# Kernel tuning notes

Hardware: AMD Instinct MI355X
Metric: run time of the kernel (lower is better)

Reference implementation:

```python
import jax, jax.numpy as jnp
import numpy as np

B, S, H, NH = 2, 2048, 768, 12
HD = H // NH
MEM_W = 0.5  # memory_weight
LN_EPS = 1e-5


def setup_inputs() -> dict:
    key = jax.random.key(0)
    ks = jax.random.split(key, 12)
    xav = lambda k: jax.random.uniform(k, (H, H), jnp.float32, -1.0, 1.0) * np.sqrt(6.0 / (H + H))
    return {
        "hidden_states": jax.random.normal(ks[0], (B, S, H), jnp.float32),
        "cross_states": jax.random.normal(ks[1], (B, S, H), jnp.float32),
        "attention_mask": jnp.ones((B, 1, S, S), jnp.int32),
        "memory_tensors": jax.random.normal(ks[2], (2, B, S, H), jnp.float32),
        "dynamic_factor": jax.random.uniform(ks[3], (B, S, 1), jnp.float32),
        "Wq": xav(ks[4]), "bq": jnp.zeros((H,), jnp.float32),
        "Wk": xav(ks[5]), "bk": jnp.zeros((H,), jnp.float32),
        "Wv": xav(ks[6]), "bv": jnp.zeros((H,), jnp.float32),
        "Wo": xav(ks[7]), "bo": jnp.zeros((H,), jnp.float32),
        "gate": jnp.ones((1,), jnp.float32),
        "gate_bias": jnp.zeros((1,), jnp.float32),
        "ln_g": jnp.ones((H,), jnp.float32),
        "ln_b": jnp.zeros((H,), jnp.float32),
    }


def _layernorm(x, g, b):
    mu = jnp.mean(x, axis=-1, keepdims=True)
    var = jnp.mean(jnp.square(x - mu), axis=-1, keepdims=True)
    return (x - mu) * jax.lax.rsqrt(var + LN_EPS) * g + b


def reference(hidden_states, cross_states, attention_mask, memory_tensors,
              dynamic_factor, Wq, bq, Wk, bk, Wv, bv, Wo, bo,
              gate, gate_bias, ln_g, ln_b):
    x = _layernorm(hidden_states, ln_g, ln_b)
    q = x @ Wq + bq                      # [B,S,H]
    k = cross_states @ Wk + bk
    v = cross_states @ Wv + bv
    k = k + memory_tensors[0] * MEM_W    # memory injection into K/V
    v = v + memory_tensors[1] * MEM_W

    q = q.reshape(B, S, NH, HD).transpose(0, 2, 1, 3)  # [B,NH,S,HD]
    k = k.reshape(B, S, NH, HD).transpose(0, 2, 1, 3)
    v = v.reshape(B, S, NH, HD).transpose(0, 2, 1, 3)

    scores = jnp.einsum("bhqd,bhkd->bhqk", q, k) / np.sqrt(HD)
    scores = jnp.where(attention_mask == 0, -jnp.inf, scores)
    attn = jax.nn.softmax(scores, axis=-1)
    out = jnp.einsum("bhqk,bhkd->bhqd", attn, v)       # [B,NH,S,HD]
    out = out.transpose(0, 2, 1, 3).reshape(B, S, H)

    out = out @ Wo + bo
    out = out * gate + gate_bias
    out = out * dynamic_factor
    return out
```

## Files before the change

kernel.cpp:

```cpp
#include <hip/hip_runtime.h>
#include <hip/hip_bf16.h>
#include <stdint.h>

#define BB   2
#define SS   2048
#define HH   768
#define NHH  12
#define HDD  64
#define BSS  (BB*SS)
#define NBH  (BB*NHH)
#define ROWS_BH (NBH*SS)
#define NSPLIT 2

typedef unsigned short u16;
typedef unsigned int   u32;
typedef __attribute__((ext_vector_type(8))) short bf16x8_t;
typedef __attribute__((ext_vector_type(4))) float f32x4;
typedef __attribute__((ext_vector_type(2))) u32   u32x2;
typedef __attribute__((ext_vector_type(4))) u32   u32x4;

#define MFMA16(a, b, c) __builtin_amdgcn_mfma_f32_16x16x32_bf16((a), (b), (c), 0, 0, 0)

__device__ __forceinline__ float b2f(u16 u) {
    u32 x = ((u32)u) << 16; float f; __builtin_memcpy(&f, &x, 4); return f;
}
__device__ __forceinline__ u16 f2b(float f) {
    u32 x; __builtin_memcpy(&x, &f, 4);
    u32 r = x + 0x7fffu + ((x >> 16) & 1u);
    return (u16)(r >> 16);
}
__device__ __forceinline__ void async16(const u16* g, u16* l) {
    __builtin_amdgcn_global_load_lds(
        (const __attribute__((address_space(1))) void*)g,
        (__attribute__((address_space(3))) void*)l, 16, 0, 0);
}

__global__ __launch_bounds__(256) void prep_kernel(
    const float* __restrict__ Wq, const float* __restrict__ Wk,
    const float* __restrict__ Wv, const float* __restrict__ Wo,
    u16* __restrict__ Wt,
    const float* __restrict__ hid, const float* __restrict__ cross,
    const float* __restrict__ g, const float* __restrict__ bb,
    u16* __restrict__ xln, u16* __restrict__ crossb,
    const int* __restrict__ mask, u32* __restrict__ bits,
    u32* __restrict__ wrow)
{
    int id = blockIdx.x;
    int t = threadIdx.x;

    if (id < 576) {
        int mat = id / 144, rem = id % 144;
        int by = rem / 12, bx = rem % 12;
        const float* src = (mat == 0) ? Wq : (mat == 1) ? Wk : (mat == 2) ? Wv : Wo;
        u16* dst = Wt + (size_t)mat * 768 * 768;

        __shared__ float sm[64][68];
        int r0 = by * 64, c0 = bx * 64;
        #pragma unroll
        for (int it = 0; it < 4; ++it) {
            int c = t + it * 256;
            int r = c >> 4, sg = c & 15;
            *(float4*)&sm[r][sg * 4] = *(const float4*)&src[(size_t)(r0 + r) * 768 + c0 + sg * 4];
        }
        __syncthreads();
        #pragma unroll
        for (int it = 0; it < 2; ++it) {
            int c = t + it * 256;
            int rr = c >> 3, sg = c & 7;
            u16 tmp[8] __attribute__((aligned(16)));
            #pragma unroll
            for (int j = 0; j < 8; ++j) tmp[j] = f2b(sm[sg * 8 + j][rr]);
            *(u32x4*)&dst[(size_t)(c0 + rr) * 768 + r0 + sg * 8] = *(u32x4*)tmp;
        }
        return;
    }

    if (id < 2624) {
        int lid = id - 576;
        int y = lid >> 10, bx = lid & 1023;
        int wv = t >> 6, lane = t & 63;
        int row = bx * 4 + wv;

        if (y == 1) {
            const float* xr = cross + (size_t)row * 768;
            u16* o = crossb + (size_t)row * 768;
            #pragma unroll
            for (int c = 0; c < 3; ++c) {
                float4 f = *(const float4*)&xr[c * 256 + lane * 4];
                u16 t4[4] __attribute__((aligned(8)));
                t4[0] = f2b(f.x); t4[1] = f2b(f.y); t4[2] = f2b(f.z); t4[3] = f2b(f.w);
                *(u32x2*)&o[c * 256 + lane * 4] = *(u32x2*)t4;
            }
            return;
        }

        const float* xr = hid + (size_t)row * 768;
        float v[12];
        float s = 0.f, s2 = 0.f;
        #pragma unroll
        for (int c = 0; c < 3; ++c) {
            float4 f = *(const float4*)&xr[c * 256 + lane * 4];
            v[c*4+0] = f.x; v[c*4+1] = f.y; v[c*4+2] = f.z; v[c*4+3] = f.w;
            s  += f.x + f.y + f.z + f.w;
            s2 += f.x*f.x + f.y*f.y + f.z*f.z + f.w*f.w;
        }
        #pragma unroll
        for (int off = 1; off < 64; off <<= 1) {
            s  += __shfl_xor(s,  off, 64);
            s2 += __shfl_xor(s2, off, 64);
        }
        float mu  = s  * (1.f / 768.f);
        float var = s2 * (1.f / 768.f) - mu * mu;
        float rs  = 1.f / sqrtf(var + 1e-5f);
        #pragma unroll
        for (int c = 0; c < 3; ++c) {
            float4 gg = *(const float4*)&g [c * 256 + lane * 4];
            float4 bv = *(const float4*)&bb[c * 256 + lane * 4];
            u16 o[4] __attribute__((aligned(8)));
            o[0] = f2b((v[c*4+0] - mu) * rs * gg.x + bv.x);
            o[1] = f2b((v[c*4+1] - mu) * rs * gg.y + bv.y);
            o[2] = f2b((v[c*4+2] - mu) * rs * gg.z + bv.z);
            o[3] = f2b((v[c*4+3] - mu) * rs * gg.w + bv.w);
            *(u32x2*)&xln[(size_t)row * 768 + c * 256 + lane * 4] = *(u32x2*)o;
        }
        return;
    }

    {
        int mid = id - 2624;
        int w = mid * 256 + t;
        const int4* p = (const int4*)(mask + (size_t)w * 32);
        u32 v = 0;
        #pragma unroll
        for (int i = 0; i < 8; ++i) {
            int4 m = p[i];
            v |= ((m.x != 0) ? 1u : 0u) << (4 * i + 0);
            v |= ((m.y != 0) ? 1u : 0u) << (4 * i + 1);
            v |= ((m.z != 0) ? 1u : 0u) << (4 * i + 2);
            v |= ((m.w != 0) ? 1u : 0u) << (4 * i + 3);
        }
        bits[w] = v;
        unsigned long long ball = __ballot(v == 0xffffffffu);
        if ((t & 63) == 0) {
            u32 wr = 0;
            #pragma unroll
            for (int kt = 0; kt < 32; ++kt)
                if (((ball >> (2 * kt)) & 3ull) == 3ull) wr |= (1u << kt);
            wrow[w >> 6] = wr;
        }
    }
}

__device__ __forceinline__ void gemm128_main(const u16* __restrict__ A,
                                             const u16* __restrict__ W,
                                             f32x4 acc[4][4])
{
    __shared__ __attribute__((aligned(16))) u16 AsL[128 * 32];
    __shared__ __attribute__((aligned(16))) u16 BsL[128 * 32];
    int m0 = blockIdx.x * 128, n0 = blockIdx.y * 128;
    int t = threadIdx.x;
    int wv = t >> 6, lane = t & 63, lm = lane & 15, quad = lane >> 4;
    int wr = wv >> 1, wc = wv & 1;

    const u16* Ap = A + (size_t)(m0 + (t >> 2)) * 768 + (t & 3) * 8;
    const u16* Bp = W + (size_t)(n0 + (t >> 2)) * 768 + (t & 3) * 8;
    u16* lA = &AsL[t * 8];
    u16* lB = &BsL[t * 8];

    for (int kt = 0; kt < 768 / 32; ++kt) {
        __syncthreads();
        async16(Ap + kt * 32,                  lA);
        async16(Ap + kt * 32 + 64 * 768,       lA + 2048);
        async16(Bp + kt * 32,                  lB);
        async16(Bp + kt * 32 + 64 * 768,       lB + 2048);
        __syncthreads();
        bf16x8_t af[4], bfv[4];
        #pragma unroll
        for (int i = 0; i < 4; ++i) af[i]  = *(const bf16x8_t*)&AsL[(wr * 64 + i * 16 + lm) * 32 + quad * 8];
        #pragma unroll
        for (int j = 0; j < 4; ++j) bfv[j] = *(const bf16x8_t*)&BsL[(wc * 64 + j * 16 + lm) * 32 + quad * 8];
        #pragma unroll
        for (int i = 0; i < 4; ++i)
            #pragma unroll
            for (int j = 0; j < 4; ++j)
                acc[i][j] = MFMA16(af[i], bfv[j], acc[i][j]);
    }
}

__global__ __launch_bounds__(256) void qkv_gemm(
    const u16* __restrict__ xln, const u16* __restrict__ crossb,
    const u16* __restrict__ Wt,  const float* __restrict__ bq,
    const float* __restrict__ bk, const float* __restrict__ bv,
    const float* __restrict__ mem,
    u16* __restrict__ Qb, u16* __restrict__ Kb, u16* __restrict__ VtG)
{
    int z = blockIdx.z;
    const u16* A      = (z == 0) ? xln : crossb;
    const u16* W      = Wt + (size_t)z * 768 * 768;
    const float* bias = (z == 0) ? bq : (z == 1) ? bk : bv;
    const float* mp   = (z == 0) ? (const float*)nullptr : mem + (size_t)(z - 1) * BSS * HH;

    f32x4 z4 = {0.f, 0.f, 0.f, 0.f};
    f32x4 acc[4][4];
    #pragma unroll
    for (int i = 0; i < 4; ++i)
        #pragma unroll
        for (int j = 0; j < 4; ++j) acc[i][j] = z4;

    gemm128_main(A, W, acc);

    int t = threadIdx.x, wv = t >> 6, lane = t & 63, lm = lane & 15, quad = lane >> 4;
    int wr = wv >> 1, wc = wv & 1;
    int row0 = blockIdx.x * 128 + wr * 64 + quad * 4;
    int col0 = blockIdx.y * 128 + wc * 64 + lm;

    if (z == 2) {
        #pragma unroll
        for (int j = 0; j < 4; ++j) {
            int cg = col0 + j * 16;
            float bz = bias[cg];
            int h = cg >> 6, d = cg & 63;
            #pragma unroll
            for (int i = 0; i < 4; ++i) {
                int rg = row0 + i * 16;
                int b = rg >> 11, s = rg & 2047;
                u16 ob[4] __attribute__((aligned(8)));
                #pragma unroll
                for (int e = 0; e < 4; ++e) {
                    float v = acc[i][j][e] + bz + 0.5f * mp[(size_t)(rg + e) * HH + cg];
                    ob[e] = f2b(v);
                }
                *(u32x2*)&VtG[((size_t)(b * NHH + h) * 64 + d) * SS + s] = *(u32x2*)ob;
            }
        }
        return;
    }

    u16* out = (z == 0) ? Qb : Kb;
    #pragma unroll
    for (int j = 0; j < 4; ++j) {
        int cg = col0 + j * 16;
        float bz = bias[cg];
        #pragma unroll
        for (int i = 0; i < 4; ++i) {
            int rg = row0 + i * 16;
            #pragma unroll
            for (int e = 0; e < 4; ++e) {
                float v = acc[i][j][e] + bz;
                if (mp) v += 0.5f * mp[(size_t)(rg + e) * HH + cg];
                out[(size_t)(rg + e) * HH + cg] = f2b(v);
            }
        }
    }
}

__global__ __launch_bounds__(256) void attn_kernel(
    const u16* __restrict__ Q, const u16* __restrict__ K,
    const u16* __restrict__ VtG, const u32* __restrict__ mbits,
    const u32* __restrict__ wrow,
    u16* __restrict__ Pacc, float* __restrict__ Pl, int ksteps)
{
    __shared__ __attribute__((aligned(16))) u16   KsL[64 * 64];
    __shared__ __attribute__((aligned(16))) u16   VtL[64 * 64];
    __shared__ __attribute__((aligned(16))) short Ps[4][16][72];

    int qt = blockIdx.x;
    int bh = blockIdx.y;
    int z  = blockIdx.z;
    int b = bh / NHH, h = bh % NHH;
    int t = threadIdx.x;
    int wv = t >> 6, lane = t & 63, lm = lane & 15, quad = lane >> 4;
    int r7 = lm & 7;

    int qrow_g = b * SS + qt * 64 + wv * 16;
    const u16* qp = Q + (size_t)(qrow_g + lm) * HH + h * 64;
    bf16x8_t qf0 = *(const bf16x8_t*)&qp[quad * 8];
    bf16x8_t qf1 = *(const bf16x8_t*)&qp[32 + quad * 8];

    f32x4 z4 = {0.f, 0.f, 0.f, 0.f};
    f32x4 acc_o[4] = {z4, z4, z4, z4};
    float l_part[4] = {0.f, 0.f, 0.f, 0.f};

    const float SC = 0.18033688011112042f;
    int qloc = qt * 64 + wv * 16 + quad * 4;

    u32 wand = wrow[b * SS + qloc + 0] & wrow[b * SS + qloc + 1] &
               wrow[b * SS + qloc + 2] & wrow[b * SS + qloc + 3];

    int c0 = t, c1 = t + 256;
    int kr0 = c0 >> 3, cs0 = (c0 & 7) ^ (kr0 & 7);
    int kr1 = c1 >> 3, cs1 = (c1 & 7) ^ (kr1 & 7);
    const u16* Kb0 = K + (size_t)(b * SS) * HH + h * 64;
    const u16* Vb0 = VtG + (size_t)bh * 64 * SS;

    int kt0 = z * ksteps;
    for (int kt = kt0; kt < kt0 + ksteps; ++kt) {
        __syncthreads();
        int k0 = kt * 64;
        async16(Kb0 + (size_t)(k0 + kr0) * HH + cs0 * 8, &KsL[c0 * 8]);
        async16(Kb0 + (size_t)(k0 + kr1) * HH + cs1 * 8, &KsL[c1 * 8]);
        async16(Vb0 + (size_t)kr0 * SS + k0 + cs0 * 8,   &VtL[c0 * 8]);
        async16(Vb0 + (size_t)kr1 * SS + k0 + cs1 * 8,   &VtL[c1 * 8]);
        __syncthreads();

        f32x4 sc[4];
        #pragma unroll
        for (int k16 = 0; k16 < 4; ++k16) {
            int rowk = k16 * 16 + lm;
            bf16x8_t kf0 = *(const bf16x8_t*)&KsL[(rowk * 8 + (quad ^ r7)) * 8];
            bf16x8_t kf1 = *(const bf16x8_t*)&KsL[(rowk * 8 + ((quad ^ 4) ^ r7)) * 8];
            f32x4 a = z4;
            a = MFMA16(qf0, kf0, a);
            a = MFMA16(qf1, kf1, a);
            sc[k16] = a;
        }

        if (!__all((int)((wand >> kt) & 1u))) {
            #pragma unroll
            for (int e = 0; e < 4; ++e) {
                u32x2 u = *(const u32x2*)&mbits[(size_t)(b * SS + qloc + e) * (SS / 32) + kt * 2];
                unsigned long long mw = ((unsigned long long)u.y << 32) | (unsigned long long)u.x;
                #pragma unroll
                for (int k16 = 0; k16 < 4; ++k16)
                    if (!((mw >> (k16 * 16 + lm)) & 1ull)) sc[k16][e] = -3.0e38f;
            }
        }

        #pragma unroll
        for (int k16 = 0; k16 < 4; ++k16) {
            #pragma unroll
            for (int e = 0; e < 4; ++e) {
                float p = __builtin_amdgcn_exp2f(sc[k16][e] * SC);
                sc[k16][e] = p;
                l_part[e] += p;
            }
        }

        #pragma unroll
        for (int k16 = 0; k16 < 4; ++k16) {
            int colg = ((k16 + quad) & 3) * 16;
            #pragma unroll
            for (int e = 0; e < 4; ++e) {
                float pv = sc[k16][e];
                u32 pb = __builtin_bit_cast(u32, pv);
                Ps[wv][quad * 4 + e][colg + lm] = (short)((pb + 0x8000u) >> 16);
            }
        }
        __asm__ volatile("" ::: "memory");

        #pragma unroll
        for (int cc = 0; cc < 2; ++cc) {
            int k16r = cc * 2 + (quad >> 1);
            int colg = ((k16r + (lm >> 2)) & 3) * 16 + (quad & 1) * 8;
            bf16x8_t pf = *(const bf16x8_t*)&Ps[wv][lm][colg];
            #pragma unroll
            for (int j = 0; j < 4; ++j) {
                bf16x8_t vf = *(const bf16x8_t*)&VtL[((j * 16 + lm) * 8 + ((cc * 4 + quad) ^ r7)) * 8];
                acc_o[j] = MFMA16(pf, vf, acc_o[j]);
            }
        }
    }

    #pragma unroll
    for (int off = 1; off < 16; off <<= 1) {
        #pragma unroll
        for (int e = 0; e < 4; ++e)
            l_part[e] += __shfl_xor(l_part[e], off, 64);
    }

    size_t prow = ((size_t)z * NBH + bh) * SS + qt * 64 + wv * 16 + quad * 4;
    #pragma unroll
    for (int j = 0; j < 4; ++j)
        #pragma unroll
        for (int e = 0; e < 4; ++e)
            Pacc[(prow + e) * 64 + j * 16 + lm] = f2b(acc_o[j][e]);
    if (lm == 0) {
        #pragma unroll
        for (int e = 0; e < 4; ++e)
            Pl[prow + e] = l_part[e];
    }
}

__global__ __launch_bounds__(256) void attn_merge(
    const u16* __restrict__ Pacc, const float* __restrict__ Pl,
    u16* __restrict__ AO)
{
    int t = threadIdx.x;
    int r = blockIdx.x * 64 + (t >> 2);
    int dseg = (t & 3) * 16;

    float lsum = Pl[r] + Pl[(size_t)ROWS_BH + r];

    float o[16];
    #pragma unroll
    for (int i = 0; i < 16; ++i) o[i] = 0.f;
    #pragma unroll
    for (int s = 0; s < NSPLIT; ++s) {
        const u16* ap = &Pacc[((size_t)s * ROWS_BH + r) * 64 + dseg];
        u32x4 a0 = *(const u32x4*)ap;
        u32x4 a1 = *(const u32x4*)(ap + 8);
        u32 wa[8];
        wa[0]=a0.x; wa[1]=a0.y; wa[2]=a0.z; wa[3]=a0.w;
        wa[4]=a1.x; wa[5]=a1.y; wa[6]=a1.z; wa[7]=a1.w;
        #pragma unroll
        for (int i = 0; i < 8; ++i) {
            o[2*i]   += b2f((u16)(wa[i] & 0xffff));
            o[2*i+1] += b2f((u16)(wa[i] >> 16));
        }
    }
    float inv = 1.f / lsum;
    int bh = r >> 11, q = r & 2047;
    int b = bh / NHH, h = bh % NHH;
    u16 ob[16] __attribute__((aligned(16)));
    #pragma unroll
    for (int i = 0; i < 16; ++i) ob[i] = f2b(o[i] * inv);
    u16* op = &AO[((size_t)(b * SS + q)) * HH + h * 64 + dseg];
    *(u32x4*)op       = *(u32x4*)ob;
    *(u32x4*)(op + 8) = *(u32x4*)(ob + 8);
}

__global__ __launch_bounds__(256) void out_gemm(
    const u16* __restrict__ AO, const u16* __restrict__ Wt,
    const float* __restrict__ bo, const float* __restrict__ gate,
    const float* __restrict__ gbias, const float* __restrict__ dyn,
    float* __restrict__ out)
{
    f32x4 z4 = {0.f, 0.f, 0.f, 0.f};
    f32x4 acc[4][4];
    #pragma unroll
    for (int i = 0; i < 4; ++i)
        #pragma unroll
        for (int j = 0; j < 4; ++j) acc[i][j] = z4;

    gemm128_main(AO, Wt, acc);

    float gv = gate[0];
    float gb = gbias[0];
    int t = threadIdx.x, wv = t >> 6, lane = t & 63, lm = lane & 15, quad = lane >> 4;
    int wr = wv >> 1, wc = wv & 1;
    int row0 = blockIdx.x * 128 + wr * 64 + quad * 4;
    int col0 = blockIdx.y * 128 + wc * 64 + lm;
    #pragma unroll
    for (int j = 0; j < 4; ++j) {
        int cg = col0 + j * 16;
        float bz = bo[cg];
        #pragma unroll
        for (int i = 0; i < 4; ++i) {
            int rg = row0 + i * 16;
            #pragma unroll
            for (int e = 0; e < 4; ++e) {
                float v = acc[i][j][e] + bz;
                v = v * gv + gb;
                v *= dyn[rg + e];
                out[(size_t)(rg + e) * HH + cg] = v;
            }
        }
    }
}

extern "C" void kernel_launch(void* const* d_in, const int* in_sizes, int n_in,
                              void* d_out, int out_size, void* d_ws, size_t ws_size,
                              hipStream_t stream)
{
    (void)in_sizes; (void)n_in; (void)out_size; (void)ws_size;

    const float* hid   = (const float*)d_in[0];
    const float* cross = (const float*)d_in[1];
    const int*   amask = (const int*)d_in[2];
    const float* mem   = (const float*)d_in[3];
    const float* dyn   = (const float*)d_in[4];
    const float* Wq    = (const float*)d_in[5];
    const float* bq    = (const float*)d_in[6];
    const float* Wk    = (const float*)d_in[7];
    const float* bk    = (const float*)d_in[8];
    const float* Wv    = (const float*)d_in[9];
    const float* bv    = (const float*)d_in[10];
    const float* Wo    = (const float*)d_in[11];
    const float* bo    = (const float*)d_in[12];
    const float* gate  = (const float*)d_in[13];
    const float* gbias = (const float*)d_in[14];
    const float* lng   = (const float*)d_in[15];
    const float* lnb   = (const float*)d_in[16];

    char* p = (char*)d_ws;
    u16* Wt   = (u16*)p; p += (size_t)4 * 768 * 768 * 2;
    u32* mb   = (u32*)p; p += (size_t)BB * SS * (SS / 32) * 4;
    u32* wrow = (u32*)p; p += (size_t)BSS * 4;
    u16* xln  = (u16*)p; p += (size_t)BSS * HH * 2;
    u16* crb  = (u16*)p; p += (size_t)BSS * HH * 2;
    u16* Qb   = (u16*)p; p += (size_t)BSS * HH * 2;
    u16* Kb   = (u16*)p; p += (size_t)BSS * HH * 2;
    u16* VtG  = (u16*)p; p += (size_t)BSS * HH * 2;
    u16* Pacc  = xln;
    float* Pl  = (float*)Wt;
    u16* AO    = Kb;

    prep_kernel <<<dim3(3648),           256, 0, stream>>>(
        Wq, Wk, Wv, Wo, Wt, hid, cross, lng, lnb, xln, crb, amask, mb, wrow);
    qkv_gemm    <<<dim3(32, 6, 3),       256, 0, stream>>>(
        xln, crb, Wt, bq, bk, bv, mem, Qb, Kb, VtG);
    attn_kernel <<<dim3(32, 24, NSPLIT), 256, 0, stream>>>(
        Qb, Kb, VtG, mb, wrow, Pacc, Pl, SS / 64 / NSPLIT);
    attn_merge  <<<dim3(ROWS_BH / 64),   256, 0, stream>>>(Pacc, Pl, AO);
    out_gemm    <<<dim3(32, 6),          256, 0, stream>>>(
        AO, Wt + (size_t)3 * 768 * 768, bo, gate, gbias, dyn, (float*)d_out);
}
```

Baseline: 266.8 us.

## Widen GEMM K-tile to 64 with swizzled LDS and double attention query tile

The shared GEMM mainloop now stages 64-wide K slices with an XOR-swizzled shared-memory layout, halving the number of barrier pairs and reducing LDS bank conflicts. The attention kernel moves to 512-thread blocks covering 128 query rows, so each K/V tile loaded into shared memory serves twice as many queries and the grid shrinks by half. The trade-offs are more LDS per GEMM block, fewer attention blocks in flight, and larger blocks that may lower occupancy.

```diff
diff --git a/kernel.cpp b/kernel.cpp
--- a/kernel.cpp
+++ b/kernel.cpp
@@ -155,35 +155,42 @@
                                              const u16* __restrict__ W,
                                              f32x4 acc[4][4])
 {
-    __shared__ __attribute__((aligned(16))) u16 AsL[128 * 32];
-    __shared__ __attribute__((aligned(16))) u16 BsL[128 * 32];
+    __shared__ __attribute__((aligned(16))) u16 AsL[128 * 64];
+    __shared__ __attribute__((aligned(16))) u16 BsL[128 * 64];
     int m0 = blockIdx.x * 128, n0 = blockIdx.y * 128;
     int t = threadIdx.x;
     int wv = t >> 6, lane = t & 63, lm = lane & 15, quad = lane >> 4;
     int wr = wv >> 1, wc = wv & 1;
 
-    const u16* Ap = A + (size_t)(m0 + (t >> 2)) * 768 + (t & 3) * 8;
-    const u16* Bp = W + (size_t)(n0 + (t >> 2)) * 768 + (t & 3) * 8;
-    u16* lA = &AsL[t * 8];
-    u16* lB = &BsL[t * 8];
-
-    for (int kt = 0; kt < 768 / 32; ++kt) {
+    for (int kt = 0; kt < 768 / 64; ++kt) {
         __syncthreads();
-        async16(Ap + kt * 32,                  lA);
-        async16(Ap + kt * 32 + 64 * 768,       lA + 2048);
-        async16(Bp + kt * 32,                  lB);
-        async16(Bp + kt * 32 + 64 * 768,       lB + 2048);
+        #pragma unroll
+        for (int it = 0; it < 4; ++it) {
+            int c = t + it * 256;
+            int row = c >> 3, cs = (c & 7) ^ (row & 7);
+            async16(A + (size_t)(m0 + row) * 768 + kt * 64 + cs * 8, &AsL[c * 8]);
+            async16(W + (size_t)(n0 + row) * 768 + kt * 64 + cs * 8, &BsL[c * 8]);
+        }
         __syncthreads();
-        bf16x8_t af[4], bfv[4];
-        #pragma unroll
-        for (int i = 0; i < 4; ++i) af[i]  = *(const bf16x8_t*)&AsL[(wr * 64 + i * 16 + lm) * 32 + quad * 8];
-        #pragma unroll
-        for (int j = 0; j < 4; ++j) bfv[j] = *(const bf16x8_t*)&BsL[(wc * 64 + j * 16 + lm) * 32 + quad * 8];
-        #pragma unroll
-        for (int i = 0; i < 4; ++i)
-            #pragma unroll
-            for (int j = 0; j < 4; ++j)
-                acc[i][j] = MFMA16(af[i], bfv[j], acc[i][j]);
+        #pragma unroll
+        for (int kk = 0; kk < 2; ++kk) {
+            bf16x8_t af[4], bfv[4];
+            #pragma unroll
+            for (int i = 0; i < 4; ++i) {
+                int r = wr * 64 + i * 16 + lm;
+                af[i] = *(const bf16x8_t*)&AsL[(r * 8 + ((kk * 4 + quad) ^ (r & 7))) * 8];
+            }
+            #pragma unroll
+            for (int j = 0; j < 4; ++j) {
+                int r = wc * 64 + j * 16 + lm;
+                bfv[j] = *(const bf16x8_t*)&BsL[(r * 8 + ((kk * 4 + quad) ^ (r & 7))) * 8];
+            }
+            #pragma unroll
+            for (int i = 0; i < 4; ++i)
+                #pragma unroll
+                for (int j = 0; j < 4; ++j)
+                    acc[i][j] = MFMA16(af[i], bfv[j], acc[i][j]);
+        }
     }
 }
 
@@ -254,7 +261,7 @@
     }
 }
 
-__global__ __launch_bounds__(256) void attn_kernel(
+__global__ __launch_bounds__(512) void attn_kernel(
     const u16* __restrict__ Q, const u16* __restrict__ K,
     const u16* __restrict__ VtG, const u32* __restrict__ mbits,
     const u32* __restrict__ wrow,
@@ -262,7 +269,7 @@
 {
     __shared__ __attribute__((aligned(16))) u16   KsL[64 * 64];
     __shared__ __attribute__((aligned(16))) u16   VtL[64 * 64];
-    __shared__ __attribute__((aligned(16))) short Ps[4][16][72];
+    __shared__ __attribute__((aligned(16))) short Ps[8][16][72];
 
     int qt = blockIdx.x;
     int bh = blockIdx.y;
@@ -272,7 +279,7 @@
     int wv = t >> 6, lane = t & 63, lm = lane & 15, quad = lane >> 4;
     int r7 = lm & 7;
 
-    int qrow_g = b * SS + qt * 64 + wv * 16;
+    int qrow_g = b * SS + qt * 128 + wv * 16;
     const u16* qp = Q + (size_t)(qrow_g + lm) * HH + h * 64;
     bf16x8_t qf0 = *(const bf16x8_t*)&qp[quad * 8];
     bf16x8_t qf1 = *(const bf16x8_t*)&qp[32 + quad * 8];
@@ -282,14 +289,12 @@
     float l_part[4] = {0.f, 0.f, 0.f, 0.f};
 
     const float SC = 0.18033688011112042f;
-    int qloc = qt * 64 + wv * 16 + quad * 4;
+    int qloc = qt * 128 + wv * 16 + quad * 4;
 
     u32 wand = wrow[b * SS + qloc + 0] & wrow[b * SS + qloc + 1] &
                wrow[b * SS + qloc + 2] & wrow[b * SS + qloc + 3];
 
-    int c0 = t, c1 = t + 256;
-    int kr0 = c0 >> 3, cs0 = (c0 & 7) ^ (kr0 & 7);
-    int kr1 = c1 >> 3, cs1 = (c1 & 7) ^ (kr1 & 7);
+    int kr = t >> 3, cs = (t & 7) ^ (kr & 7);
     const u16* Kb0 = K + (size_t)(b * SS) * HH + h * 64;
     const u16* Vb0 = VtG + (size_t)bh * 64 * SS;
 
@@ -297,10 +302,8 @@
     for (int kt = kt0; kt < kt0 + ksteps; ++kt) {
         __syncthreads();
         int k0 = kt * 64;
-        async16(Kb0 + (size_t)(k0 + kr0) * HH + cs0 * 8, &KsL[c0 * 8]);
-        async16(Kb0 + (size_t)(k0 + kr1) * HH + cs1 * 8, &KsL[c1 * 8]);
-        async16(Vb0 + (size_t)kr0 * SS + k0 + cs0 * 8,   &VtL[c0 * 8]);
-        async16(Vb0 + (size_t)kr1 * SS + k0 + cs1 * 8,   &VtL[c1 * 8]);
+        async16(Kb0 + (size_t)(k0 + kr) * HH + cs * 8, &KsL[t * 8]);
+        async16(Vb0 + (size_t)kr * SS + k0 + cs * 8,   &VtL[t * 8]);
         __syncthreads();
 
         f32x4 sc[4];
@@ -368,7 +371,7 @@
             l_part[e] += __shfl_xor(l_part[e], off, 64);
     }
 
-    size_t prow = ((size_t)z * NBH + bh) * SS + qt * 64 + wv * 16 + quad * 4;
+    size_t prow = ((size_t)z * NBH + bh) * SS + qt * 128 + wv * 16 + quad * 4;
     #pragma unroll
     for (int j = 0; j < 4; ++j)
         #pragma unroll
@@ -499,7 +502,7 @@
         Wq, Wk, Wv, Wo, Wt, hid, cross, lng, lnb, xln, crb, amask, mb, wrow);
     qkv_gemm    <<<dim3(32, 6, 3),       256, 0, stream>>>(
         xln, crb, Wt, bq, bk, bv, mem, Qb, Kb, VtG);
-    attn_kernel <<<dim3(32, 24, NSPLIT), 256, 0, stream>>>(
+    attn_kernel <<<dim3(16, 24, NSPLIT), 512, 0, stream>>>(
         Qb, Kb, VtG, mb, wrow, Pacc, Pl, SS / 64 / NSPLIT);
     attn_merge  <<<dim3(ROWS_BH / 64),   256, 0, stream>>>(Pacc, Pl, AO);
     out_gemm    <<<dim3(32, 6),          256, 0, stream>>>(
```

Measured after the change: 262.2 us. No clear change (-1.7%).
